# Kernel optimization log

Measured on AMD Instinct MI355X. Metric: run time of the kernel, lower is better.

Reference implementation:

```python
import jax, jax.numpy as jnp
import numpy as np

D_MODEL, D_MLP, D_HEAD, N_HEADS, SEQ, BATCH = 1024, 4096, 64, 16, 2048, 2


def setup_inputs() -> dict:
    key = jax.random.key(0)
    ks = jax.random.split(key, 7)
    s = 1.0 / np.sqrt(D_MODEL)
    return {
        "x": jax.random.normal(ks[0], (BATCH, SEQ, D_MODEL), jnp.float32),
        "W_K": jax.random.normal(ks[1], (N_HEADS, D_HEAD, D_MODEL), jnp.float32) * s,
        "W_Q": jax.random.normal(ks[2], (N_HEADS, D_HEAD, D_MODEL), jnp.float32) * s,
        "W_V": jax.random.normal(ks[3], (N_HEADS, D_HEAD, D_MODEL), jnp.float32) * s,
        "W_O": jax.random.normal(ks[4], (D_MODEL, N_HEADS * D_HEAD), jnp.float32) * s,
        "W_in": jax.random.normal(ks[5], (D_MLP, D_MODEL), jnp.float32) * s,
        "b_in": jnp.zeros((D_MLP,), jnp.float32),
        "W_out": jax.random.normal(ks[6], (D_MODEL, D_MLP), jnp.float32) * s,
        "b_out": jnp.zeros((D_MODEL,), jnp.float32),
    }


def _block(x, W_K, W_Q, W_V, W_O, W_in, b_in, W_out, b_out):
    S = x.shape[-2]
    # attention
    k = jnp.einsum('ihd,bpd->biph', W_K, x)
    q = jnp.einsum('ihd,bpd->biph', W_Q, x)
    v = jnp.einsum('ihd,bpd->biph', W_V, x)
    scores = jnp.einsum('biph,biqh->biqp', k, q)  # [B,H,S(query q),S(key p)]
    causal = jnp.tril(jnp.ones((S, S), x.dtype))
    masked = jnp.tril(scores) - 1e10 * (1.0 - causal)
    attn = jax.nn.softmax(masked / np.sqrt(D_HEAD), axis=-1)
    z = jnp.einsum('biph,biqp->biqh', v, attn)  # [B,H,S,d_head]
    z_flat = jnp.transpose(z, (0, 2, 1, 3)).reshape(x.shape[0], S, -1)  # b q (i h)
    attn_out = jnp.einsum('df,bqf->bqd', W_O, z_flat)
    x = x + attn_out
    # MLP
    h = jax.nn.relu(jnp.einsum('md,bpd->bpm', W_in, x) + b_in)
    x = x + jnp.einsum('dm,bpm->bpd', W_out, h) + b_out
    return x


def reference(x, W_K, W_Q, W_V, W_O, W_in, b_in, W_out, b_out):
    return _block(x, W_K, W_Q, W_V, W_O, W_in, b_in, W_out, b_out)
```

## Files before the change

kernel.cpp:

```cpp
#include <hip/hip_runtime.h>

typedef unsigned short u16;
typedef __bf16 bf16x8 __attribute__((ext_vector_type(8)));
typedef float f32x4 __attribute__((ext_vector_type(4)));
typedef u16 u16x8 __attribute__((ext_vector_type(8), may_alias));
typedef u16 u16x4 __attribute__((ext_vector_type(4), may_alias));
typedef unsigned int u32x4 __attribute__((ext_vector_type(4)));

#define D_MODEL 1024
#define D_MLP   4096
#define D_HEAD  64
#define N_HEADS 16
#define SEQ     2048
#define BATCH   2
#define BS      (BATCH * SEQ)
#define QKV_N   3072
#define QSCALE  0.18033688011112042f

__device__ __forceinline__ u16 f2b(float f) {
  unsigned u = __builtin_bit_cast(unsigned, f);
  u += 0x7fffu + ((u >> 16) & 1u);
  return (u16)(u >> 16);
}

__device__ __forceinline__ unsigned cvtpk_bf16(float lo, float hi) {
  unsigned r;
  asm("v_cvt_pk_bf16_f32 %0, %1, %2" : "=v"(r) : "v"(lo), "v"(hi));
  return r;
}

__device__ __forceinline__ void gload_lds16(const u16* g, u16* l) {
  __builtin_amdgcn_global_load_lds(
      (const __attribute__((address_space(1))) unsigned int*)g,
      (__attribute__((address_space(3))) unsigned int*)l, 16, 0, 0);
}

__global__ __launch_bounds__(256) void cvt_kernel(const float* __restrict__ in,
                                                  u16* __restrict__ out, int n4) {
  int i = blockIdx.x * 256 + threadIdx.x;
  if (i >= n4) return;
  float4 v = ((const float4*)in)[i];
  u16x4 o;
  o[0] = f2b(v.x); o[1] = f2b(v.y); o[2] = f2b(v.z); o[3] = f2b(v.w);
  ((u16x4*)out)[i] = o;
}

template<int MODE>
__global__ __launch_bounds__(256) void gemm_bt(
    const u16* __restrict__ A, const u16* __restrict__ Bw,
    int M, int N, int K,
    u16* __restrict__ outb, float* __restrict__ outf,
    const float* __restrict__ resid, const float* __restrict__ bias,
    u16* __restrict__ vtp, int gx)
{
  __shared__ u16 Asm_[128 * 64];
  __shared__ u16 Bsm_[128 * 64];
  const int t = threadIdx.x;
  const int lane = t & 63;
  const int l15 = lane & 15, l4 = lane >> 4;
  const int w = t >> 6;
  const int wr = w >> 1, wc = w & 1;

  const int xcd = blockIdx.x & 7;
  const int local = blockIdx.x >> 3;
  const int rw = gx >> 2;
  const int rx = xcd & 3, ry = xcd >> 2;
  const int c = local >> 4, r0 = local & 15;
  int bx = rx * rw + c;
  const int by = ry * 16 + r0;
  int z = 0;
  if (MODE == 3) { z = bx >> 3; bx &= 7; }
  const int m0 = by * 128;
  const int n0 = bx * 128;
  const int kb = (MODE == 3) ? z * (K >> 1) : 0;
  const int ke = (MODE == 3) ? kb + (K >> 1) : K;

  f32x4 acc[4][4] = {};

  for (int k0 = kb; k0 < ke; k0 += 64) {
    __syncthreads();
#pragma unroll
    for (int i = 0; i < 4; ++i) {
      int s = i * 256 + t;
      int row = s >> 3;
      int sl = s & 7;
      int gc = ((sl ^ (row & 7)) << 3);
      const u16* ga = A + (size_t)(m0 + row) * K + (k0 + gc);
      const u16* gb = Bw + (size_t)(n0 + row) * K + (k0 + gc);
      u16* la = Asm_ + (i * 256 + (t & ~63)) * 8;
      u16* lb = Bsm_ + (i * 256 + (t & ~63)) * 8;
      gload_lds16(ga, la);
      gload_lds16(gb, lb);
    }
    asm volatile("s_waitcnt vmcnt(0)" ::: "memory");
    __syncthreads();
#pragma unroll
    for (int kk = 0; kk < 2; ++kk) {
      bf16x8 af[4], bfr[4];
#pragma unroll
      for (int mi = 0; mi < 4; ++mi) {
        int row = wr * 64 + mi * 16 + l15;
        int sl2 = (kk * 4 + l4) ^ (row & 7);
        u16x8 ua = *(const u16x8*)(Asm_ + row * 64 + sl2 * 8);
        af[mi] = __builtin_bit_cast(bf16x8, ua);
      }
#pragma unroll
      for (int ni = 0; ni < 4; ++ni) {
        int row = wc * 64 + ni * 16 + l15;
        int sl2 = (kk * 4 + l4) ^ (row & 7);
        u16x8 ub = *(const u16x8*)(Bsm_ + row * 64 + sl2 * 8);
        bfr[ni] = __builtin_bit_cast(bf16x8, ub);
      }
#pragma unroll
      for (int mi = 0; mi < 4; ++mi)
#pragma unroll
        for (int ni = 0; ni < 4; ++ni)
          acc[mi][ni] = __builtin_amdgcn_mfma_f32_16x16x32_bf16(af[mi], bfr[ni], acc[mi][ni], 0, 0, 0);
    }
  }

#pragma unroll
  for (int mi = 0; mi < 4; ++mi) {
    int rowb = m0 + wr * 64 + mi * 16 + l4 * 4;
#pragma unroll
    for (int ni = 0; ni < 4; ++ni) {
      int col = n0 + wc * 64 + ni * 16 + l15;
#pragma unroll
      for (int r = 0; r < 4; ++r) {
        float v = acc[mi][ni][r];
        int row = rowb + r;
        if (MODE == 0) {
          if (col < 2048) {
            float o = (col < 1024) ? v * QSCALE : v;
            outb[((size_t)row << 11) + col] = f2b(o);
          } else {
            int c2 = col - 2048;
            size_t vi = (((size_t)((row >> 11) * 1024 + c2)) << 11) + (row & (SEQ - 1));
            vtp[vi] = f2b(v);
          }
        } else if (MODE == 3) {
          outf[(size_t)z * M * N + (size_t)row * N + col] = v;
        } else {
          size_t idx = (size_t)row * N + col;
          if (MODE == 1) {
            float o = v + resid[idx];
            outf[idx] = o;
            outb[idx] = f2b(o);
          } else {
            float o = v + bias[col];
            o = o > 0.f ? o : 0.f;
            outb[idx] = f2b(o);
          }
        }
      }
    }
  }
}

__global__ __launch_bounds__(256) void reduce2_kernel(const float* __restrict__ part,
                                                      const float* __restrict__ resid,
                                                      const float* __restrict__ bias,
                                                      float* __restrict__ out) {
  const int i = blockIdx.x * 256 + threadIdx.x;
  float4 a = ((const float4*)part)[i];
  float4 b = ((const float4*)(part + (size_t)BS * D_MODEL))[i];
  float4 r = ((const float4*)resid)[i];
  float4 bi = ((const float4*)bias)[i & 255];
  float4 o;
  o.x = a.x + b.x + r.x + bi.x;
  o.y = a.y + b.y + r.y + bi.y;
  o.z = a.z + b.z + r.z + bi.z;
  o.w = a.w + b.w + r.w + bi.w;
  ((float4*)out)[i] = o;
}

__global__ __launch_bounds__(256) void attn_kernel(const u16* __restrict__ qk,
                                                   const u16* __restrict__ vT,
                                                   u16* __restrict__ zb)
{
  __shared__ u16 Kl[2][64 * 64];
  __shared__ u16 Vl[2][64 * 72];
  const int t = threadIdx.x;
  const int w = t >> 6;
  const int lane = t & 63;
  const int l15 = lane & 15, l4 = lane >> 4;
  const int blk = blockIdx.x;
  const int bh = blk & 31;
  const int qb = 15 - (blk >> 5);
  const int b = bh >> 4, h = bh & 15;
  const int q0w = qb * 128 + w * 32;
  const int myLastT = (4 * qb + w) >> 1;
  const int ttmaxB = 2 * qb + 1;

  bf16x8 qf[2][2];
#pragma unroll
  for (int s = 0; s < 2; ++s) {
    const u16* qp = qk + (((size_t)(b * SEQ + q0w + s * 16 + l15)) << 11) + h * 64 + l4 * 8;
    qf[s][0] = __builtin_bit_cast(bf16x8, *(const u16x8*)(qp));
    qf[s][1] = __builtin_bit_cast(bf16x8, *(const u16x8*)(qp + 32));
  }

  const int srow = t >> 3;
  const int sgc = ((t & 7) ^ (srow & 7)) * 8;
  const u16* kgbase = qk + (((size_t)(b * SEQ + srow)) << 11) + 1024 + h * 64 + sgc;
  u16* kldst = &Kl[0][0] + (t & ~63) * 8;
  const int vd2 = t >> 2, q4 = t & 3;
  const u16* vgbase = vT + (((size_t)(bh * 64 + vd2)) << 11);

  f32x4 zacc[2][4] = {};
  float m_run[2] = {-1e30f, -1e30f}, l_run[2] = {0.f, 0.f};

  auto compute = [&](int buf, int tt) {
    bf16x8 kf[4][2];
#pragma unroll
    for (int ks = 0; ks < 4; ++ks) {
      int row = ks * 16 + l15;
#pragma unroll
      for (int kc = 0; kc < 2; ++kc) {
        int slot = (kc * 4 + l4) ^ (row & 7);
        kf[ks][kc] = __builtin_bit_cast(bf16x8, *(const u16x8*)&Kl[buf][row * 64 + slot * 8]);
      }
    }
    bf16x8 vf[2][4];
#pragma unroll
    for (int g = 0; g < 2; ++g)
#pragma unroll
      for (int dn = 0; dn < 4; ++dn)
        vf[g][dn] = __builtin_bit_cast(bf16x8,
            *(const u16x8*)&Vl[buf][(dn * 16 + l15) * 72 + g * 32 + l4 * 8]);

    const bool last = (tt == myLastT);
#pragma unroll
    for (int s = 0; s < 2; ++s) {
      f32x4 sf[4] = {};
      __builtin_amdgcn_s_setprio(1);
#pragma unroll
      for (int ks = 0; ks < 4; ++ks) {
        sf[ks] = __builtin_amdgcn_mfma_f32_16x16x32_bf16(kf[ks][0], qf[s][0], sf[ks], 0, 0, 0);
        sf[ks] = __builtin_amdgcn_mfma_f32_16x16x32_bf16(kf[ks][1], qf[s][1], sf[ks], 0, 0, 0);
      }
      __builtin_amdgcn_s_setprio(0);

      if (last) {
        const int qq = q0w + s * 16 + l15;
        const int pb = tt * 64 + l4 * 4;
#pragma unroll
        for (int ks = 0; ks < 4; ++ks)
#pragma unroll
          for (int r = 0; r < 4; ++r)
            sf[ks][r] = (pb + ks * 16 + r <= qq) ? sf[ks][r] : -1e30f;
      }

      float mk[4];
#pragma unroll
      for (int ks = 0; ks < 4; ++ks)
        mk[ks] = fmaxf(fmaxf(sf[ks][0], sf[ks][1]), fmaxf(sf[ks][2], sf[ks][3]));
      float mt = fmaxf(fmaxf(mk[0], mk[1]), fmaxf(mk[2], mk[3]));
      mt = fmaxf(mt, __shfl_xor(mt, 16));
      mt = fmaxf(mt, __shfl_xor(mt, 32));
      const float mn = fmaxf(m_run[s], mt);
      const float sc = __builtin_amdgcn_exp2f(m_run[s] - mn);
      m_run[s] = mn;
      float pv[4][4];
      float rs = 0.f;
#pragma unroll
      for (int ks = 0; ks < 4; ++ks)
#pragma unroll
        for (int r = 0; r < 4; ++r) {
          pv[ks][r] = __builtin_amdgcn_exp2f(sf[ks][r] - mn);
          rs += pv[ks][r];
        }
      rs += __shfl_xor(rs, 16);
      rs += __shfl_xor(rs, 32);
      l_run[s] = l_run[s] * sc + rs;

#pragma unroll
      for (int dn = 0; dn < 4; ++dn)
#pragma unroll
        for (int r = 0; r < 4; ++r) zacc[s][dn][r] *= sc;

      bf16x8 pa[2];
#pragma unroll
      for (int g = 0; g < 2; ++g) {
        u32x4 pu;
        pu[0] = cvtpk_bf16(pv[2 * g][0], pv[2 * g][1]);
        pu[1] = cvtpk_bf16(pv[2 * g][2], pv[2 * g][3]);
        pu[2] = cvtpk_bf16(pv[2 * g + 1][0], pv[2 * g + 1][1]);
        pu[3] = cvtpk_bf16(pv[2 * g + 1][2], pv[2 * g + 1][3]);
        pa[g] = __builtin_bit_cast(bf16x8, pu);
      }

      __builtin_amdgcn_s_setprio(1);
#pragma unroll
      for (int dn = 0; dn < 4; ++dn) {
        zacc[s][dn] = __builtin_amdgcn_mfma_f32_16x16x32_bf16(vf[0][dn], pa[0], zacc[s][dn], 0, 0, 0);
        zacc[s][dn] = __builtin_amdgcn_mfma_f32_16x16x32_bf16(vf[1][dn], pa[1], zacc[s][dn], 0, 0, 0);
      }
      __builtin_amdgcn_s_setprio(0);
    }
  };

  gload_lds16(kgbase, kldst);
  gload_lds16(kgbase + ((size_t)1 << 16), kldst + 2048);
  {
    const u16* vg = vgbase;
    u16x4 a0 = *(const u16x4*)(vg + q4 * 4);
    u16x4 a1 = *(const u16x4*)(vg + 16 + q4 * 4);
    u16x4 b0 = *(const u16x4*)(vg + 32 + q4 * 4);
    u16x4 b1 = *(const u16x4*)(vg + 48 + q4 * 4);
    *(u16x8*)&Vl[0][vd2 * 72 + q4 * 8] =
        __builtin_shufflevector(a0, a1, 0, 1, 2, 3, 4, 5, 6, 7);
    *(u16x8*)&Vl[0][vd2 * 72 + 32 + q4 * 8] =
        __builtin_shufflevector(b0, b1, 0, 1, 2, 3, 4, 5, 6, 7);
  }
  asm volatile("s_waitcnt vmcnt(0)" ::: "memory");
  __syncthreads();

  int cur = 0;
  for (int tt = 0; tt <= ttmaxB; ++tt) {
    const bool more = tt < ttmaxB;
    u16x4 a0, a1, b0, b1;
    if (more) {
      const u16* kg = kgbase + ((size_t)(tt + 1) << 17);
      u16* kld = kldst + (cur ^ 1) * 4096;
      gload_lds16(kg, kld);
      gload_lds16(kg + ((size_t)1 << 16), kld + 2048);
      const u16* vg = vgbase + (tt + 1) * 64;
      a0 = *(const u16x4*)(vg + q4 * 4);
      a1 = *(const u16x4*)(vg + 16 + q4 * 4);
      b0 = *(const u16x4*)(vg + 32 + q4 * 4);
      b1 = *(const u16x4*)(vg + 48 + q4 * 4);
    }
    if (tt <= myLastT) compute(cur, tt);
    if (more) {
      *(u16x8*)&Vl[cur ^ 1][vd2 * 72 + q4 * 8] =
          __builtin_shufflevector(a0, a1, 0, 1, 2, 3, 4, 5, 6, 7);
      *(u16x8*)&Vl[cur ^ 1][vd2 * 72 + 32 + q4 * 8] =
          __builtin_shufflevector(b0, b1, 0, 1, 2, 3, 4, 5, 6, 7);
    }
    asm volatile("s_waitcnt vmcnt(0)" ::: "memory");
    __syncthreads();
    cur ^= 1;
  }

#pragma unroll
  for (int s = 0; s < 2; ++s) {
    const float inv = 1.f / l_run[s];
    const size_t rowoff = ((size_t)(b * SEQ + q0w + s * 16 + l15)) * D_MODEL + h * 64 + l4 * 4;
#pragma unroll
    for (int dn = 0; dn < 4; ++dn) {
      u16x4 o;
#pragma unroll
      for (int r = 0; r < 4; ++r) o[r] = f2b(zacc[s][dn][r] * inv);
      *(u16x4*)(zb + rowoff + dn * 16) = o;
    }
  }
}

extern "C" void kernel_launch(void* const* d_in, const int* in_sizes, int n_in,
                              void* d_out, int out_size, void* d_ws, size_t ws_size,
                              hipStream_t stream) {
  const float* x     = (const float*)d_in[0];
  const float* W_K   = (const float*)d_in[1];
  const float* W_Q   = (const float*)d_in[2];
  const float* W_V   = (const float*)d_in[3];
  const float* W_O   = (const float*)d_in[4];
  const float* W_in  = (const float*)d_in[5];
  const float* b_in  = (const float*)d_in[6];
  const float* W_out = (const float*)d_in[7];
  const float* b_out = (const float*)d_in[8];
  float* out = (float*)d_out;

  char* p = (char*)d_ws;
  u16* xb    = (u16*)p;            p += (size_t)BS * D_MODEL * 2;
  u16* wqkv  = (u16*)p;            p += (size_t)QKV_N * D_MODEL * 2;
  u16* wo_b  = (u16*)p;            p += (size_t)D_MODEL * D_MODEL * 2;
  u16* win_b = (u16*)p;            p += (size_t)D_MLP * D_MODEL * 2;
  u16* wout_b= (u16*)p;            p += (size_t)D_MODEL * D_MLP * 2;
  float* x1f = (float*)p;          p += (size_t)BS * D_MODEL * 4;
  u16* hb    = (u16*)p;            p += (size_t)BS * D_MLP * 2;
  u16* qk    = (u16*)p;            p += (size_t)BS * 2048 * 2;
  u16* vt    = (u16*)p;            p += (size_t)BATCH * 1024 * SEQ * 2;
  u16* zb    = (u16*)p;            p += (size_t)BS * D_MODEL * 2;
  u16* x1b   = (u16*)p;            p += (size_t)BS * D_MODEL * 2;
  float* part = (float*)qk;

  auto cvt = [&](const float* src, u16* dst, int n) {
    int n4 = n / 4;
    cvt_kernel<<<(n4 + 255) / 256, 256, 0, stream>>>(src, dst, n4);
  };
  cvt(x, xb, BS * D_MODEL);
  cvt(W_Q, wqkv + 0,                  N_HEADS * D_HEAD * D_MODEL);
  cvt(W_K, wqkv + 1024 * 1024,        N_HEADS * D_HEAD * D_MODEL);
  cvt(W_V, wqkv + 2 * 1024 * 1024,    N_HEADS * D_HEAD * D_MODEL);
  cvt(W_O, wo_b,  D_MODEL * D_MODEL);
  cvt(W_in, win_b, D_MLP * D_MODEL);
  cvt(W_out, wout_b, D_MODEL * D_MLP);

  gemm_bt<0><<<dim3(24 * 32), 256, 0, stream>>>(
      xb, wqkv, BS, QKV_N, D_MODEL, qk, nullptr, nullptr, nullptr, vt, 24);

  attn_kernel<<<dim3(512), 256, 0, stream>>>(qk, vt, zb);

  gemm_bt<1><<<dim3(8 * 32), 256, 0, stream>>>(
      zb, wo_b, BS, D_MODEL, D_MODEL, x1b, x1f, x, nullptr, nullptr, 8);

  gemm_bt<2><<<dim3(32 * 32), 256, 0, stream>>>(
      x1b, win_b, BS, D_MLP, D_MODEL, hb, nullptr, nullptr, b_in, nullptr, 32);

  gemm_bt<3><<<dim3(16 * 32), 256, 0, stream>>>(
      hb, wout_b, BS, D_MODEL, D_MLP, nullptr, part, nullptr, nullptr, nullptr, 16);

  reduce2_kernel<<<dim3(BS * D_MODEL / 4 / 256), 256, 0, stream>>>(part, x1f, b_out, out);
}
```

Measured before the change: 269.1 us.

## Split causal attention over key segments with separate log-sum-exp merge kernel

The attention kernel now splits each 128-row query block's key range into segments of 8 key tiles, giving 40 work units per batch-head instead of 16 blocks of uneven length. Each unit writes unnormalized fp32 partial outputs plus its running max and sum into reused workspace buffers. A new merge kernel rescales and combines the partials and writes the bf16 output. This balances load across CUs and raises occupancy, at the cost of an extra launch and extra fp32 partial traffic.

Result: slower. 278.7 us (+3.6%).

```diff
diff --git a/kernel.cpp b/kernel.cpp
--- a/kernel.cpp
+++ b/kernel.cpp
@@ -16,6 +16,7 @@
 #define BS      (BATCH * SEQ)
 #define QKV_N   3072
 #define QSCALE  0.18033688011112042f
+#define NSEG_TOTAL 40
 
 __device__ __forceinline__ u16 f2b(float f) {
   unsigned u = __builtin_bit_cast(unsigned, f);
@@ -176,7 +177,8 @@
 
 __global__ __launch_bounds__(256) void attn_kernel(const u16* __restrict__ qk,
                                                    const u16* __restrict__ vT,
-                                                   u16* __restrict__ zb)
+                                                   float* __restrict__ zpart,
+                                                   float* __restrict__ ml)
 {
   __shared__ u16 Kl[2][64 * 64];
   __shared__ u16 Vl[2][64 * 72];
@@ -186,11 +188,16 @@
   const int l15 = lane & 15, l4 = lane >> 4;
   const int blk = blockIdx.x;
   const int bh = blk & 31;
-  const int qb = 15 - (blk >> 5);
+  const int u = (NSEG_TOTAL - 1) - (blk >> 5);
+  int qb = 0, cc = 0;
+  while (cc + ((qb >> 2) + 1) <= u) { cc += (qb >> 2) + 1; ++qb; }
+  const int seg = u - cc;
+  const int NSm1 = qb >> 2;
   const int b = bh >> 4, h = bh & 15;
   const int q0w = qb * 128 + w * 32;
   const int myLastT = (4 * qb + w) >> 1;
-  const int ttmaxB = 2 * qb + 1;
+  const int ptbeg = seg * 8;
+  const int ttendB = (seg == NSm1) ? (2 * qb + 1) : (ptbeg + 7);
 
   bf16x8 qf[2][2];
 #pragma unroll
@@ -300,10 +307,10 @@
     }
   };
 
-  gload_lds16(kgbase, kldst);
-  gload_lds16(kgbase + ((size_t)1 << 16), kldst + 2048);
+  gload_lds16(kgbase + ((size_t)ptbeg << 17), kldst);
+  gload_lds16(kgbase + ((size_t)ptbeg << 17) + ((size_t)1 << 16), kldst + 2048);
   {
-    const u16* vg = vgbase;
+    const u16* vg = vgbase + ptbeg * 64;
     u16x4 a0 = *(const u16x4*)(vg + q4 * 4);
     u16x4 a1 = *(const u16x4*)(vg + 16 + q4 * 4);
     u16x4 b0 = *(const u16x4*)(vg + 32 + q4 * 4);
@@ -317,8 +324,8 @@
   __syncthreads();
 
   int cur = 0;
-  for (int tt = 0; tt <= ttmaxB; ++tt) {
-    const bool more = tt < ttmaxB;
+  for (int tt = ptbeg; tt <= ttendB; ++tt) {
+    const bool more = tt < ttendB;
     u16x4 a0, a1, b0, b1;
     if (more) {
       const u16* kg = kgbase + ((size_t)(tt + 1) << 17);
@@ -343,17 +350,58 @@
     cur ^= 1;
   }
 
+  const int slot = u * 32 + bh;
+  float* zp = zpart + (size_t)slot * (128 * 64);
+  float* mlp = ml + (size_t)slot * 256;
 #pragma unroll
   for (int s = 0; s < 2; ++s) {
-    const float inv = 1.f / l_run[s];
-    const size_t rowoff = ((size_t)(b * SEQ + q0w + s * 16 + l15)) * D_MODEL + h * 64 + l4 * 4;
-#pragma unroll
-    for (int dn = 0; dn < 4; ++dn) {
-      u16x4 o;
-#pragma unroll
-      for (int r = 0; r < 4; ++r) o[r] = f2b(zacc[s][dn][r] * inv);
-      *(u16x4*)(zb + rowoff + dn * 16) = o;
-    }
+    const int qrow = 32 * w + s * 16 + l15;
+#pragma unroll
+    for (int dn = 0; dn < 4; ++dn)
+      *(f32x4*)(zp + qrow * 64 + dn * 16 + l4 * 4) = zacc[s][dn];
+    if (l4 == 0) {
+      mlp[qrow * 2 + 0] = m_run[s];
+      mlp[qrow * 2 + 1] = l_run[s];
+    }
+  }
+}
+
+__global__ __launch_bounds__(256) void attn_merge(const float* __restrict__ zpart,
+                                                  const float* __restrict__ ml,
+                                                  u16* __restrict__ zb)
+{
+  const int blk = blockIdx.x;
+  const int bh = blk & 31, qb = blk >> 5;
+  const int b = bh >> 4, h = bh & 15;
+  const int a = qb >> 2, bq = qb & 3;
+  const int C = 2 * a * (a + 1) + bq * (a + 1);
+  const int NS = a + 1;
+  const float* zp0 = zpart + ((size_t)(C * 32 + bh)) * (128 * 64);
+  const float* ml0 = ml + ((size_t)(C * 32 + bh)) * 256;
+
+  for (int k = 0; k < 8; ++k) {
+    const int e4 = threadIdx.x + k * 256;
+    const int q = e4 >> 4;
+    float mg = -1e30f;
+    for (int s2 = 0; s2 < NS; ++s2)
+      mg = fmaxf(mg, ml0[s2 * (32 * 256) + q * 2]);
+    float den = 0.f;
+    float4 num = {0.f, 0.f, 0.f, 0.f};
+    for (int s2 = 0; s2 < NS; ++s2) {
+      const float mm = ml0[s2 * (32 * 256) + q * 2];
+      const float ll = ml0[s2 * (32 * 256) + q * 2 + 1];
+      const float wgt = __builtin_amdgcn_exp2f(mm - mg);
+      den += wgt * ll;
+      float4 zv = ((const float4*)(zp0 + (size_t)s2 * (32 * 128 * 64)))[e4];
+      num.x += wgt * zv.x; num.y += wgt * zv.y;
+      num.z += wgt * zv.z; num.w += wgt * zv.w;
+    }
+    const float inv = 1.f / den;
+    const int d4 = e4 & 15;
+    u16x4 o;
+    o[0] = f2b(num.x * inv); o[1] = f2b(num.y * inv);
+    o[2] = f2b(num.z * inv); o[3] = f2b(num.w * inv);
+    *(u16x4*)(zb + ((size_t)(b * SEQ + qb * 128 + q)) * D_MODEL + h * 64 + d4 * 4) = o;
   }
 }
 
@@ -384,6 +432,8 @@
   u16* zb    = (u16*)p;            p += (size_t)BS * D_MODEL * 2;
   u16* x1b   = (u16*)p;            p += (size_t)BS * D_MODEL * 2;
   float* part = (float*)qk;
+  float* zpart = x1f;
+  float* mlbuf = (float*)wqkv;
 
   auto cvt = [&](const float* src, u16* dst, int n) {
     int n4 = n / 4;
@@ -400,7 +450,8 @@
   gemm_bt<0><<<dim3(24 * 32), 256, 0, stream>>>(
       xb, wqkv, BS, QKV_N, D_MODEL, qk, nullptr, nullptr, nullptr, vt, 24);
 
-  attn_kernel<<<dim3(512), 256, 0, stream>>>(qk, vt, zb);
+  attn_kernel<<<dim3(32 * NSEG_TOTAL), 256, 0, stream>>>(qk, vt, zpart, mlbuf);
+  attn_merge<<<dim3(512), 256, 0, stream>>>(zpart, mlbuf, zb);
 
   gemm_bt<1><<<dim3(8 * 32), 256, 0, stream>>>(
       zb, wo_b, BS, D_MODEL, D_MODEL, x1b, x1f, x, nullptr, nullptr, 8);
```

## Process 128-key tiles per attention iteration with inline LDS fragment loads

Applied to the files above, without the earlier changes.

Doubles the attention key/value tile from 64 to 128 keys per loop iteration, halving loop iterations and barrier/synchronization overhead. K and V fragments are read from LDS just before each MFMA instead of being preloaded into registers, which cuts register pressure. In exchange LDS usage roughly doubles, which may lower occupancy. All waves now process the full diagonal tile, adding some masked work.

Result: faster. 255.4 us (-5.1%).

```diff
diff --git a/kernel.cpp b/kernel.cpp
--- a/kernel.cpp
+++ b/kernel.cpp
@@ -178,8 +178,8 @@
                                                    const u16* __restrict__ vT,
                                                    u16* __restrict__ zb)
 {
-  __shared__ u16 Kl[2][64 * 64];
-  __shared__ u16 Vl[2][64 * 72];
+  __shared__ u16 Kl[2][128 * 64];
+  __shared__ u16 Vl[2][64 * 136];
   const int t = threadIdx.x;
   const int w = t >> 6;
   const int lane = t & 63;
@@ -189,8 +189,7 @@
   const int qb = 15 - (blk >> 5);
   const int b = bh >> 4, h = bh & 15;
   const int q0w = qb * 128 + w * 32;
-  const int myLastT = (4 * qb + w) >> 1;
-  const int ttmaxB = 2 * qb + 1;
+  const int ttmax = qb;
 
   bf16x8 qf[2][2];
 #pragma unroll
@@ -210,61 +209,58 @@
   f32x4 zacc[2][4] = {};
   float m_run[2] = {-1e30f, -1e30f}, l_run[2] = {0.f, 0.f};
 
+  auto stageK = [&](int buf, int tt) {
+    const u16* kg = kgbase + ((size_t)tt << 18);
+    u16* kld = kldst + buf * (128 * 64);
+#pragma unroll
+    for (int i = 0; i < 4; ++i)
+      gload_lds16(kg + ((size_t)i << 16), kld + i * 2048);
+  };
+
   auto compute = [&](int buf, int tt) {
-    bf16x8 kf[4][2];
-#pragma unroll
-    for (int ks = 0; ks < 4; ++ks) {
-      int row = ks * 16 + l15;
-#pragma unroll
-      for (int kc = 0; kc < 2; ++kc) {
-        int slot = (kc * 4 + l4) ^ (row & 7);
-        kf[ks][kc] = __builtin_bit_cast(bf16x8, *(const u16x8*)&Kl[buf][row * 64 + slot * 8]);
-      }
-    }
-    bf16x8 vf[2][4];
-#pragma unroll
-    for (int g = 0; g < 2; ++g)
-#pragma unroll
-      for (int dn = 0; dn < 4; ++dn)
-        vf[g][dn] = __builtin_bit_cast(bf16x8,
-            *(const u16x8*)&Vl[buf][(dn * 16 + l15) * 72 + g * 32 + l4 * 8]);
-
-    const bool last = (tt == myLastT);
+    const bool last = (tt == ttmax);
 #pragma unroll
     for (int s = 0; s < 2; ++s) {
-      f32x4 sf[4] = {};
+      f32x4 sf[8] = {};
       __builtin_amdgcn_s_setprio(1);
 #pragma unroll
-      for (int ks = 0; ks < 4; ++ks) {
-        sf[ks] = __builtin_amdgcn_mfma_f32_16x16x32_bf16(kf[ks][0], qf[s][0], sf[ks], 0, 0, 0);
-        sf[ks] = __builtin_amdgcn_mfma_f32_16x16x32_bf16(kf[ks][1], qf[s][1], sf[ks], 0, 0, 0);
+      for (int ks = 0; ks < 8; ++ks) {
+        const int row = ks * 16 + l15;
+#pragma unroll
+        for (int kc = 0; kc < 2; ++kc) {
+          const int slot = (kc * 4 + l4) ^ (row & 7);
+          bf16x8 kf = __builtin_bit_cast(bf16x8,
+              *(const u16x8*)&Kl[buf][row * 64 + slot * 8]);
+          sf[ks] = __builtin_amdgcn_mfma_f32_16x16x32_bf16(kf, qf[s][kc], sf[ks], 0, 0, 0);
+        }
       }
       __builtin_amdgcn_s_setprio(0);
 
       if (last) {
         const int qq = q0w + s * 16 + l15;
-        const int pb = tt * 64 + l4 * 4;
-#pragma unroll
-        for (int ks = 0; ks < 4; ++ks)
+        const int pb = tt * 128 + l4 * 4;
+#pragma unroll
+        for (int ks = 0; ks < 8; ++ks)
 #pragma unroll
           for (int r = 0; r < 4; ++r)
             sf[ks][r] = (pb + ks * 16 + r <= qq) ? sf[ks][r] : -1e30f;
       }
 
-      float mk[4];
-#pragma unroll
-      for (int ks = 0; ks < 4; ++ks)
+      float mk[8];
+#pragma unroll
+      for (int ks = 0; ks < 8; ++ks)
         mk[ks] = fmaxf(fmaxf(sf[ks][0], sf[ks][1]), fmaxf(sf[ks][2], sf[ks][3]));
-      float mt = fmaxf(fmaxf(mk[0], mk[1]), fmaxf(mk[2], mk[3]));
+      float mt = fmaxf(fmaxf(fmaxf(mk[0], mk[1]), fmaxf(mk[2], mk[3])),
+                       fmaxf(fmaxf(mk[4], mk[5]), fmaxf(mk[6], mk[7])));
       mt = fmaxf(mt, __shfl_xor(mt, 16));
       mt = fmaxf(mt, __shfl_xor(mt, 32));
       const float mn = fmaxf(m_run[s], mt);
       const float sc = __builtin_amdgcn_exp2f(m_run[s] - mn);
       m_run[s] = mn;
-      float pv[4][4];
+      float pv[8][4];
       float rs = 0.f;
 #pragma unroll
-      for (int ks = 0; ks < 4; ++ks)
+      for (int ks = 0; ks < 8; ++ks)
 #pragma unroll
         for (int r = 0; r < 4; ++r) {
           pv[ks][r] = __builtin_amdgcn_exp2f(sf[ks][r] - mn);
@@ -279,64 +275,59 @@
 #pragma unroll
         for (int r = 0; r < 4; ++r) zacc[s][dn][r] *= sc;
 
-      bf16x8 pa[2];
-#pragma unroll
-      for (int g = 0; g < 2; ++g) {
+      __builtin_amdgcn_s_setprio(1);
+#pragma unroll
+      for (int g = 0; g < 4; ++g) {
         u32x4 pu;
         pu[0] = cvtpk_bf16(pv[2 * g][0], pv[2 * g][1]);
         pu[1] = cvtpk_bf16(pv[2 * g][2], pv[2 * g][3]);
         pu[2] = cvtpk_bf16(pv[2 * g + 1][0], pv[2 * g + 1][1]);
         pu[3] = cvtpk_bf16(pv[2 * g + 1][2], pv[2 * g + 1][3]);
-        pa[g] = __builtin_bit_cast(bf16x8, pu);
-      }
-
-      __builtin_amdgcn_s_setprio(1);
-#pragma unroll
-      for (int dn = 0; dn < 4; ++dn) {
-        zacc[s][dn] = __builtin_amdgcn_mfma_f32_16x16x32_bf16(vf[0][dn], pa[0], zacc[s][dn], 0, 0, 0);
-        zacc[s][dn] = __builtin_amdgcn_mfma_f32_16x16x32_bf16(vf[1][dn], pa[1], zacc[s][dn], 0, 0, 0);
+        const bf16x8 pa = __builtin_bit_cast(bf16x8, pu);
+#pragma unroll
+        for (int dn = 0; dn < 4; ++dn) {
+          bf16x8 vfr = __builtin_bit_cast(bf16x8,
+              *(const u16x8*)&Vl[buf][(dn * 16 + l15) * 136 + g * 32 + l4 * 8]);
+          zacc[s][dn] = __builtin_amdgcn_mfma_f32_16x16x32_bf16(vfr, pa, zacc[s][dn], 0, 0, 0);
+        }
       }
       __builtin_amdgcn_s_setprio(0);
     }
   };
 
-  gload_lds16(kgbase, kldst);
-  gload_lds16(kgbase + ((size_t)1 << 16), kldst + 2048);
+  stageK(0, 0);
   {
-    const u16* vg = vgbase;
-    u16x4 a0 = *(const u16x4*)(vg + q4 * 4);
-    u16x4 a1 = *(const u16x4*)(vg + 16 + q4 * 4);
-    u16x4 b0 = *(const u16x4*)(vg + 32 + q4 * 4);
-    u16x4 b1 = *(const u16x4*)(vg + 48 + q4 * 4);
-    *(u16x8*)&Vl[0][vd2 * 72 + q4 * 8] =
-        __builtin_shufflevector(a0, a1, 0, 1, 2, 3, 4, 5, 6, 7);
-    *(u16x8*)&Vl[0][vd2 * 72 + 32 + q4 * 8] =
-        __builtin_shufflevector(b0, b1, 0, 1, 2, 3, 4, 5, 6, 7);
+#pragma unroll
+    for (int g = 0; g < 4; ++g) {
+      const u16* vg = vgbase + g * 32 + q4 * 4;
+      u16x4 lo = *(const u16x4*)(vg);
+      u16x4 hi = *(const u16x4*)(vg + 16);
+      *(u16x8*)&Vl[0][vd2 * 136 + g * 32 + q4 * 8] =
+          __builtin_shufflevector(lo, hi, 0, 1, 2, 3, 4, 5, 6, 7);
+    }
   }
   asm volatile("s_waitcnt vmcnt(0)" ::: "memory");
   __syncthreads();
 
   int cur = 0;
-  for (int tt = 0; tt <= ttmaxB; ++tt) {
-    const bool more = tt < ttmaxB;
-    u16x4 a0, a1, b0, b1;
+  for (int tt = 0; tt <= ttmax; ++tt) {
+    const bool more = tt < ttmax;
+    u16x4 lo[4], hi[4];
     if (more) {
-      const u16* kg = kgbase + ((size_t)(tt + 1) << 17);
-      u16* kld = kldst + (cur ^ 1) * 4096;
-      gload_lds16(kg, kld);
-      gload_lds16(kg + ((size_t)1 << 16), kld + 2048);
-      const u16* vg = vgbase + (tt + 1) * 64;
-      a0 = *(const u16x4*)(vg + q4 * 4);
-      a1 = *(const u16x4*)(vg + 16 + q4 * 4);
-      b0 = *(const u16x4*)(vg + 32 + q4 * 4);
-      b1 = *(const u16x4*)(vg + 48 + q4 * 4);
-    }
-    if (tt <= myLastT) compute(cur, tt);
+      stageK(cur ^ 1, tt + 1);
+#pragma unroll
+      for (int g = 0; g < 4; ++g) {
+        const u16* vg = vgbase + (tt + 1) * 128 + g * 32 + q4 * 4;
+        lo[g] = *(const u16x4*)(vg);
+        hi[g] = *(const u16x4*)(vg + 16);
+      }
+    }
+    compute(cur, tt);
     if (more) {
-      *(u16x8*)&Vl[cur ^ 1][vd2 * 72 + q4 * 8] =
-          __builtin_shufflevector(a0, a1, 0, 1, 2, 3, 4, 5, 6, 7);
-      *(u16x8*)&Vl[cur ^ 1][vd2 * 72 + 32 + q4 * 8] =
-          __builtin_shufflevector(b0, b1, 0, 1, 2, 3, 4, 5, 6, 7);
+#pragma unroll
+      for (int g = 0; g < 4; ++g)
+        *(u16x8*)&Vl[cur ^ 1][vd2 * 136 + g * 32 + q4 * 8] =
+            __builtin_shufflevector(lo[g], hi[g], 0, 1, 2, 3, 4, 5, 6, 7);
     }
     asm volatile("s_waitcnt vmcnt(0)" ::: "memory");
     __syncthreads();
```
